# Performance work log

Hardware: AMD Instinct MI355X
Metric: run time of the kernel (lower is better)

Reference implementation:

```python
import jax, jax.numpy as jnp
import numpy as np

E = 64          # num_expert
DIN = 512       # d_input
DOUT = 512      # d_output
T = 131072      # total routed tokens (sum of fwd_expert_count)


def setup_inputs() -> dict:
    key = jax.random.key(0)
    k1, k2, k3 = jax.random.split(key, 3)
    inp = jax.random.normal(k1, (T, DIN), dtype=jnp.float32)
    # FMoELinear params: weight [E, d_out, d_in], bias [E, d_out]
    weight = jax.random.normal(k2, (E, DOUT, DIN), dtype=jnp.float32) * (1.0 / np.sqrt(DIN))
    bias = jax.random.normal(k3, (E, DOUT), dtype=jnp.float32) * 0.01
    # Irregular per-expert token counts summing exactly to T (host-side int64,
    # as in fastmoe where fwd_expert_count lives on CPU and drives dispatch).
    rng = np.random.default_rng(0)
    counts = rng.multinomial(T, np.full(E, 1.0 / E))
    fwd_expert_count = np.asarray(counts, dtype=np.int64)
    return {"inp": inp, "weight": weight, "bias": bias, "fwd_expert_count": fwd_expert_count}


def reference(inp, weight, bias, fwd_expert_count):
    # Grouped GEMM: tokens are sorted by expert; expert e owns rows
    # [offs[e], offs[e+1]).  y_i = x_i @ W_e^T + b_e.
    counts = np.asarray(fwd_expert_count)
    offs = np.concatenate([[0], np.cumsum(counts)])
    outs = []
    for e in range(counts.shape[0]):  # fixed small loop over experts
        xe = inp[int(offs[e]):int(offs[e + 1])]          # [n_e, d_in]
        outs.append(xe @ weight[e].T + bias[e])          # [n_e, d_out]
    return jnp.concatenate(outs, axis=0)                 # [T, d_out]
```

## Files before the change

kernel.cpp:

```cpp
#include <hip/hip_runtime.h>
#include <hip/hip_bf16.h>
#include <stdint.h>

#define NE    64
#define DIN   512
#define DOUT  512
#define TTOK  131072
#define BM    128
#define BN    128
#define BK    64
#define NKSTEP (DIN / BK)
#define TILES_TOTAL (TTOK / BM + NE)
#define NXCD  8
#define TPX   (TILES_TOTAL / NXCD)

typedef __bf16 bf16x8_t __attribute__((ext_vector_type(8)));
typedef __bf16 bf16x4_t __attribute__((ext_vector_type(4)));
typedef float  f32x4_t  __attribute__((ext_vector_type(4)));

__global__ void setup_tiles(const int* __restrict__ cnt, int* __restrict__ ws) {
    int e = threadIdx.x;
    if (e >= NE) return;
    int off = 0, tbase = 0;
    for (int i = 0; i < e; ++i) {
        int c = cnt[i];
        off += c;
        tbase += (c + (BM - 1)) / BM;
    }
    int c = cnt[e];
    int nt = (c + (BM - 1)) / BM;
    int* tbl = ws + 4;
    for (int t = 0; t < nt; ++t) {
        int idx = tbase + t;
        tbl[4 * idx + 0] = e;
        tbl[4 * idx + 1] = off + t * BM;
        tbl[4 * idx + 2] = off + c;
        tbl[4 * idx + 3] = 0;
    }
    if (e == NE - 1) ws[0] = tbase + nt;
}

__global__ __launch_bounds__(256, 3) void moe_gemm(
    const float* __restrict__ inp,
    const float* __restrict__ weight,
    const float* __restrict__ bias,
    const int* __restrict__ ws,
    float* __restrict__ out)
{
    __shared__ __align__(16) unsigned char lds[2 * BM * BK * 2];

    const int bid  = blockIdx.x;
    const int xcd  = bid & (NXCD - 1);
    const int slot = bid >> 3;
    const int tile = xcd * TPX + (slot >> 2);
    const int n0   = (slot & 3) * BN;

    const int ntiles = ws[0];
    if (tile >= ntiles) return;
    const int4 ti = ((const int4*)(ws + 4))[tile];
    const int e = ti.x, row0 = ti.y, row_end = ti.z;

    const int tid  = threadIdx.x;
    const int lane = tid & 63;
    const int wave = tid >> 6;
    const int wr = (wave >> 1) * 64;
    const int wc = (wave & 1) * 64;

    const int srow = tid >> 4;
    const int sc4  = tid & 15;

    const float* __restrict__ aptr = inp + (size_t)row0 * DIN + sc4 * 4;
    const float* __restrict__ bptr = weight + (size_t)e * (DOUT * DIN)
                                     + (size_t)n0 * DIN + sc4 * 4;

    f32x4_t ra[8], rb[8];

    auto loadg = [&](int kk) {
        const int k0 = kk * BK;
#pragma unroll
        for (int i = 0; i < 8; ++i) {
            const int row = srow + i * 16;
            if (row0 + row < row_end) {
                ra[i] = *(const f32x4_t*)(aptr + (size_t)row * DIN + k0);
            } else {
                f32x4_t z = {0.f, 0.f, 0.f, 0.f};
                ra[i] = z;
            }
            rb[i] = *(const f32x4_t*)(bptr + (size_t)row * DIN + k0);
        }
    };

    auto lds_addr = [&](int which, int row, int kbyte) -> unsigned char* {
        return &lds[which * 16384 + row * 128 + (kbyte ^ ((row & 7) << 4))];
    };

    auto store_lds = [&]() {
#pragma unroll
        for (int i = 0; i < 8; ++i) {
            const int row = srow + i * 16;
            bf16x4_t ha, hb;
#pragma unroll
            for (int j = 0; j < 4; ++j) {
                ha[j] = (__bf16)ra[i][j];
                hb[j] = (__bf16)rb[i][j];
            }
            *(bf16x4_t*)lds_addr(0, row, sc4 * 8) = ha;
            *(bf16x4_t*)lds_addr(1, row, sc4 * 8) = hb;
        }
    };

    f32x4_t acc[4][4] = {};

    const int frow = lane & 15;
    const int fkb  = (lane >> 4) * 16;

    auto compute = [&]() {
#pragma unroll
        for (int ks = 0; ks < 2; ++ks) {
            bf16x8_t af[4], bg[4];
#pragma unroll
            for (int m = 0; m < 4; ++m)
                af[m] = *(const bf16x8_t*)lds_addr(0, wr + m * 16 + frow, ks * 64 + fkb);
#pragma unroll
            for (int n = 0; n < 4; ++n)
                bg[n] = *(const bf16x8_t*)lds_addr(1, wc + n * 16 + frow, ks * 64 + fkb);
#pragma unroll
            for (int m = 0; m < 4; ++m)
#pragma unroll
                for (int n = 0; n < 4; ++n)
                    acc[m][n] = __builtin_amdgcn_mfma_f32_16x16x32_bf16(
                        af[m], bg[n], acc[m][n], 0, 0, 0);
        }
    };

    loadg(0);
    store_lds();
    __syncthreads();
#pragma unroll 1
    for (int kk = 0; kk < NKSTEP - 1; ++kk) {
        loadg(kk + 1);
        __builtin_amdgcn_sched_barrier(0);
        compute();
        __syncthreads();
        store_lds();
        __syncthreads();
    }
    compute();

    const int crow = (lane >> 4) * 4;
    const int ccol = lane & 15;
    float bv[4];
#pragma unroll
    for (int n = 0; n < 4; ++n)
        bv[n] = bias[e * DOUT + n0 + wc + n * 16 + ccol];
#pragma unroll
    for (int m = 0; m < 4; ++m) {
#pragma unroll
        for (int j = 0; j < 4; ++j) {
            const int grow = row0 + wr + m * 16 + crow + j;
            if (grow < row_end) {
                float* orow = out + (size_t)grow * DOUT + n0 + wc + ccol;
#pragma unroll
                for (int n = 0; n < 4; ++n)
                    orow[n * 16] = acc[m][n][j] + bv[n];
            }
        }
    }
}

extern "C" void kernel_launch(void* const* d_in, const int* in_sizes, int n_in,
                              void* d_out, int out_size, void* d_ws, size_t ws_size,
                              hipStream_t stream) {
    const float* inp    = (const float*)d_in[0];
    const float* weight = (const float*)d_in[1];
    const float* bias   = (const float*)d_in[2];
    const int* cnt      = (const int*)d_in[3];
    float* out = (float*)d_out;
    int* ws = (int*)d_ws;

    hipLaunchKernelGGL(setup_tiles, dim3(1), dim3(64), 0, stream, cnt, ws);
    hipLaunchKernelGGL(moe_gemm, dim3(TILES_TOTAL * 4), dim3(256), 0, stream,
                       inp, weight, bias, ws, out);
}
```

Baseline: 222.6 us.

## Stream fp32 A tiles to LDS with direct global-to-LDS loads and triple buffering

Reworks the GEMM main loop. Each block grows to a 256-row tile with 512 threads and BK=32. The fp32 activation tile is loaded straight into LDS with global_load_lds into a three-stage ring buffer, and converted to bf16 only when fragments are read. Weights still pass through registers into a double-buffered bf16 LDS tile. The change adds manual waitcnt and barrier scheduling plus setprio around the MFMAs, aiming to overlap memory traffic with compute and cut register-staging overhead. In exchange it uses much more LDS (112 KB), which lowers occupancy, and does more conversion work per fragment read.

```diff
diff --git a/kernel.cpp b/kernel.cpp
--- a/kernel.cpp
+++ b/kernel.cpp
@@ -6,10 +6,10 @@
 #define DIN   512
 #define DOUT  512
 #define TTOK  131072
-#define BM    128
+#define BM    256
 #define BN    128
-#define BK    64
-#define NKSTEP (DIN / BK)
+#define BK    32
+#define NK    (DIN / BK)
 #define TILES_TOTAL (TTOK / BM + NE)
 #define NXCD  8
 #define TPX   (TILES_TOTAL / NXCD)
@@ -17,6 +17,10 @@
 typedef __bf16 bf16x8_t __attribute__((ext_vector_type(8)));
 typedef __bf16 bf16x4_t __attribute__((ext_vector_type(4)));
 typedef float  f32x4_t  __attribute__((ext_vector_type(4)));
+
+#define LDS_BYTES 114688
+#define ABUF(i) ((i) * 32768)
+#define BBUF(i) (98304 + (i) * 8192)
 
 __global__ void setup_tiles(const int* __restrict__ cnt, int* __restrict__ ws) {
     int e = threadIdx.x;
@@ -40,14 +44,20 @@
     if (e == NE - 1) ws[0] = tbase + nt;
 }
 
-__global__ __launch_bounds__(256, 3) void moe_gemm(
+__device__ __forceinline__ void gload16(const float* g, uint8_t* l) {
+    __builtin_amdgcn_global_load_lds(
+        (const __attribute__((address_space(1))) uint32_t*)g,
+        (__attribute__((address_space(3))) uint32_t*)l, 16, 0, 0);
+}
+
+__global__ __launch_bounds__(512, 2) void moe_gemm(
     const float* __restrict__ inp,
     const float* __restrict__ weight,
     const float* __restrict__ bias,
     const int* __restrict__ ws,
     float* __restrict__ out)
 {
-    __shared__ __align__(16) unsigned char lds[2 * BM * BK * 2];
+    __shared__ __align__(16) uint8_t smem[LDS_BYTES];
 
     const int bid  = blockIdx.x;
     const int xcd  = bid & (NXCD - 1);
@@ -63,92 +73,109 @@
     const int tid  = threadIdx.x;
     const int lane = tid & 63;
     const int wave = tid >> 6;
+
+    const int dr = lane >> 3;
+    const int ac = lane & 7;
+    const float* asrc[4];
+#pragma unroll
+    for (int i = 0; i < 4; ++i) {
+        int arow = wave * 32 + i * 8 + dr;
+        int grow = row0 + arow;
+        if (grow > row_end - 1) grow = row_end - 1;
+        asrc[i] = inp + (size_t)grow * DIN + ((ac ^ dr) << 2);
+    }
+
+    const int brow = tid >> 2;
+    const int bc2  = (tid & 3) * 2;
+    const float* bsrc = weight + (size_t)e * (DOUT * DIN)
+                        + (size_t)(n0 + brow) * DIN + bc2 * 4;
+    const int bwoff0 = brow * 64 + ((bc2 * 8)     ^ ((brow & 3) << 4));
+    const int bwoff1 = brow * 64 + ((bc2 * 8 + 8) ^ ((brow & 3) << 4));
+
+    f32x4_t rb[2];
+    auto issueB = [&](int kk) {
+        rb[0] = *(const f32x4_t*)(bsrc + kk * BK);
+        rb[1] = *(const f32x4_t*)(bsrc + kk * BK + 4);
+    };
+    auto issueA = [&](int kk, int buf) {
+        uint8_t* dst = smem + ABUF(buf) + wave * 4096;
+#pragma unroll
+        for (int i = 0; i < 4; ++i)
+            gload16(asrc[i] + kk * BK, dst + i * 1024);
+    };
+    auto writeB = [&](int buf) {
+        bf16x4_t h0, h1;
+#pragma unroll
+        for (int j = 0; j < 4; ++j) {
+            h0[j] = (__bf16)rb[0][j];
+            h1[j] = (__bf16)rb[1][j];
+        }
+        *(bf16x4_t*)(smem + BBUF(buf) + bwoff0) = h0;
+        *(bf16x4_t*)(smem + BBUF(buf) + bwoff1) = h1;
+    };
+
     const int wr = (wave >> 1) * 64;
     const int wc = (wave & 1) * 64;
-
-    const int srow = tid >> 4;
-    const int sc4  = tid & 15;
-
-    const float* __restrict__ aptr = inp + (size_t)row0 * DIN + sc4 * 4;
-    const float* __restrict__ bptr = weight + (size_t)e * (DOUT * DIN)
-                                     + (size_t)n0 * DIN + sc4 * 4;
-
-    f32x4_t ra[8], rb[8];
-
-    auto loadg = [&](int kk) {
-        const int k0 = kk * BK;
-#pragma unroll
-        for (int i = 0; i < 8; ++i) {
-            const int row = srow + i * 16;
-            if (row0 + row < row_end) {
-                ra[i] = *(const f32x4_t*)(aptr + (size_t)row * DIN + k0);
-            } else {
-                f32x4_t z = {0.f, 0.f, 0.f, 0.f};
-                ra[i] = z;
+    const int frow = lane & 15;
+    const int kg   = lane >> 4;
+
+    f32x4_t acc[4][4] = {};
+
+    auto compute = [&](int abuf, int bbuf) {
+        bf16x8_t af[4], bg[4];
+#pragma unroll
+        for (int m = 0; m < 4; ++m) {
+            const int row = wr + m * 16 + frow;
+            const uint8_t* p = smem + ABUF(abuf) + row * 128;
+            const int sw = (row & 7) << 4;
+            f32x4_t q0 = *(const f32x4_t*)(p + ((kg * 32)      ^ sw));
+            f32x4_t q1 = *(const f32x4_t*)(p + ((kg * 32 + 16) ^ sw));
+#pragma unroll
+            for (int j = 0; j < 4; ++j) {
+                af[m][j]     = (__bf16)q0[j];
+                af[m][4 + j] = (__bf16)q1[j];
             }
-            rb[i] = *(const f32x4_t*)(bptr + (size_t)row * DIN + k0);
-        }
-    };
-
-    auto lds_addr = [&](int which, int row, int kbyte) -> unsigned char* {
-        return &lds[which * 16384 + row * 128 + (kbyte ^ ((row & 7) << 4))];
-    };
-
-    auto store_lds = [&]() {
-#pragma unroll
-        for (int i = 0; i < 8; ++i) {
-            const int row = srow + i * 16;
-            bf16x4_t ha, hb;
-#pragma unroll
-            for (int j = 0; j < 4; ++j) {
-                ha[j] = (__bf16)ra[i][j];
-                hb[j] = (__bf16)rb[i][j];
-            }
-            *(bf16x4_t*)lds_addr(0, row, sc4 * 8) = ha;
-            *(bf16x4_t*)lds_addr(1, row, sc4 * 8) = hb;
-        }
-    };
-
-    f32x4_t acc[4][4] = {};
-
-    const int frow = lane & 15;
-    const int fkb  = (lane >> 4) * 16;
-
-    auto compute = [&]() {
-#pragma unroll
-        for (int ks = 0; ks < 2; ++ks) {
-            bf16x8_t af[4], bg[4];
-#pragma unroll
-            for (int m = 0; m < 4; ++m)
-                af[m] = *(const bf16x8_t*)lds_addr(0, wr + m * 16 + frow, ks * 64 + fkb);
+        }
+#pragma unroll
+        for (int n = 0; n < 4; ++n) {
+            const int row = wc + n * 16 + frow;
+            bg[n] = *(const bf16x8_t*)(smem + BBUF(bbuf) + row * 64
+                                       + ((kg * 16) ^ ((row & 3) << 4)));
+        }
+        __builtin_amdgcn_s_setprio(1);
+#pragma unroll
+        for (int m = 0; m < 4; ++m)
 #pragma unroll
             for (int n = 0; n < 4; ++n)
-                bg[n] = *(const bf16x8_t*)lds_addr(1, wc + n * 16 + frow, ks * 64 + fkb);
-#pragma unroll
-            for (int m = 0; m < 4; ++m)
-#pragma unroll
-                for (int n = 0; n < 4; ++n)
-                    acc[m][n] = __builtin_amdgcn_mfma_f32_16x16x32_bf16(
-                        af[m], bg[n], acc[m][n], 0, 0, 0);
-        }
-    };
-
-    loadg(0);
-    store_lds();
-    __syncthreads();
-#pragma unroll 1
-    for (int kk = 0; kk < NKSTEP - 1; ++kk) {
-        loadg(kk + 1);
-        __builtin_amdgcn_sched_barrier(0);
-        compute();
-        __syncthreads();
-        store_lds();
-        __syncthreads();
-    }
-    compute();
-
-    const int crow = (lane >> 4) * 4;
-    const int ccol = lane & 15;
+                acc[m][n] = __builtin_amdgcn_mfma_f32_16x16x32_bf16(
+                    af[m], bg[n], acc[m][n], 0, 0, 0);
+        __builtin_amdgcn_s_setprio(0);
+    };
+
+    issueB(0);
+    issueA(0, 0);
+    issueA(1, 1);
+    writeB(0);
+    asm volatile("s_waitcnt vmcnt(4)" ::: "memory");
+    __builtin_amdgcn_sched_barrier(0);
+    asm volatile("s_waitcnt lgkmcnt(0)" ::: "memory");
+    __builtin_amdgcn_s_barrier();
+
+#pragma unroll
+    for (int k = 0; k < NK; ++k) {
+        if (k + 1 < NK) issueB(k + 1);
+        if (k + 2 < NK) issueA(k + 2, (k + 2) % 3);
+        compute(k % 3, k & 1);
+        if (k + 1 < NK) {
+            writeB((k + 1) & 1);
+            asm volatile("s_waitcnt lgkmcnt(0)" ::: "memory");
+            __builtin_amdgcn_sched_barrier(0);
+            __builtin_amdgcn_s_barrier();
+        }
+    }
+
+    const int crow = kg * 4;
+    const int ccol = frow;
     float bv[4];
 #pragma unroll
     for (int n = 0; n < 4; ++n)
@@ -179,6 +206,6 @@
     int* ws = (int*)d_ws;
 
     hipLaunchKernelGGL(setup_tiles, dim3(1), dim3(64), 0, stream, cnt, ws);
-    hipLaunchKernelGGL(moe_gemm, dim3(TILES_TOTAL * 4), dim3(256), 0, stream,
+    hipLaunchKernelGGL(moe_gemm, dim3(TILES_TOTAL * 4), dim3(512), 0, stream,
                        inp, weight, bias, ws, out);
 }
```

New measurement: 270.2 us. 21.4% more time.
